# Kernel optimization log

Measured on AMD Instinct MI355X. Metric: run time of the kernel, lower is better.

Reference implementation:

```python
import jax, jax.numpy as jnp
import numpy as np

ALPHA = 0.1        # axis_aligned_projection threshold
NEG_INF = -1e30    # large negative used for masking (softmax-equivalent to -inf)


def axis_aligned_projection(x, alpha=ALPHA):
    x_abs = jnp.abs(x)
    max_vals = jnp.max(x_abs, axis=-1, keepdims=True)
    axis_weights = jnp.where(x_abs >= alpha * max_vals, x_abs, 0.0)
    return axis_weights * jnp.sign(x)


def setup_inputs() -> dict:
    key = jax.random.key(0)
    kq, kk, kv = jax.random.split(key, 3)
    B, L, H, E = 4, 2048, 8, 64
    S, D = L, E
    queries = jax.random.normal(kq, (B, L, H, E), dtype=jnp.float32)
    keys = jax.random.normal(kk, (B, S, H, E), dtype=jnp.float32)
    values = jax.random.normal(kv, (B, S, H, D), dtype=jnp.float32)
    # TriangularCausalMask: True strictly above the diagonal -> masked out
    causal = jnp.triu(jnp.ones((L, S), dtype=jnp.bool_), k=1)
    attn_mask = jnp.broadcast_to(causal[None, None], (B, 1, L, S))
    return {"queries": queries, "keys": keys, "values": values, "attn_mask": attn_mask}


def reference(queries, keys, values, attn_mask):
    B, L, H, E = queries.shape
    scale = 1.0 / jnp.sqrt(jnp.float32(E))
    q = axis_aligned_projection(queries)
    k = axis_aligned_projection(keys)
    # [B,H,L,S] dense scores (the module materializes the full matrix)
    scores = jnp.einsum('blhe,bshe->bhls', q, k)
    scores = jnp.where(attn_mask, NEG_INF, scores)
    A = jax.nn.softmax(scale * scores, axis=-1)  # dropout is identity in eval mode
    V = jnp.einsum('bhls,bshd->blhd', A, values)
    return V
```

## Files before the change

kernel.cpp:

```cpp
#include <hip/hip_runtime.h>
#include <hip/hip_bf16.h>
#include <stdint.h>

#define B_ 4
#define L_ 2048
#define H_ 8
#define E_ 64
#define ALPHA 0.1f
#define LOG2E 1.44269504088896f
#define QSCALE (0.125f * LOG2E)


typedef float f32x4 __attribute__((ext_vector_type(4)));
typedef short bf16x8 __attribute__((ext_vector_type(8)));
typedef short bf16x4 __attribute__((ext_vector_type(4)));
typedef uint32_t u32;
typedef unsigned short u16;
typedef u32 u32x2 __attribute__((ext_vector_type(2)));

__device__ __forceinline__ u16 f2bf(float f) {
    u32 x = __builtin_bit_cast(u32, f);
    u32 r = x + 0x7fffu + ((x >> 16) & 1u);
    return (u16)(r >> 16);
}

__device__ __forceinline__ u32 pk2bf(float a, float b) {
    u32 ua = __builtin_bit_cast(u32, a) + 0x8000u;
    u32 ub = __builtin_bit_cast(u32, b) + 0x8000u;
    return (ua >> 16) | (ub & 0xffff0000u);
}

__device__ __forceinline__ f32x4 mfma16x16x16bf16(bf16x4 a, bf16x4 b, f32x4 c) {
#if __has_builtin(__builtin_amdgcn_mfma_f32_16x16x16bf16_1k)
    return __builtin_amdgcn_mfma_f32_16x16x16bf16_1k(a, b, c, 0, 0, 0);
#elif __has_builtin(__builtin_amdgcn_mfma_f32_16x16x16_bf16)
    return __builtin_amdgcn_mfma_f32_16x16x16_bf16(a, b, c, 0, 0, 0);
#else
    f32x4 d;
    asm volatile("v_mfma_f32_16x16x16_bf16 %0, %1, %2, %3"
                 : "=v"(d) : "v"(a), "v"(b), "v"(c));
    return d;
#endif
}

__device__ __forceinline__ void dma16(const u16* g, u16* l) {
    __builtin_amdgcn_global_load_lds(
        (const __attribute__((address_space(1))) void*)g,
        (__attribute__((address_space(3))) void*)l, 16, 0, 0);
}

__global__ __launch_bounds__(256) void prep_kernel(const float* __restrict__ qin,
                                                   const float* __restrict__ kin,
                                                   const float* __restrict__ vin,
                                                   u16* __restrict__ qp,
                                                   u16* __restrict__ kp,
                                                   u16* __restrict__ vt) {
    __shared__ u16 tile[64][66];
    if (blockIdx.x < 4096) {
        const int RG = (B_ * L_ * H_) / 8;
        int wave = threadIdx.x >> 6, lane = threadIdx.x & 63;
        int g = blockIdx.x * 4 + wave;
        const float* src;
        u16* dst;
        int gr;
        float sc;
        bool isq;
        if (g < RG) { src = qin; dst = qp; gr = g; sc = QSCALE; isq = true; }
        else        { src = kin; dst = kp; gr = g - RG; sc = 1.0f; isq = false; }

        int rig = lane >> 3;
        int j = lane & 7;
        int c = j * 4;
        int row = gr * 8 + rig;

        const float* rp = src + (size_t)row * 64;
        float4 v0 = *(const float4*)(rp + c);
        float4 v1 = *(const float4*)(rp + c + 32);
        float f[8] = {v0.x, v0.y, v0.z, v0.w, v1.x, v1.y, v1.z, v1.w};

        float mx = 0.f;
#pragma unroll
        for (int i = 0; i < 8; ++i) mx = fmaxf(mx, fabsf(f[i]));
#pragma unroll
        for (int m = 1; m < 8; m <<= 1) mx = fmaxf(mx, __shfl_xor(mx, m));
        float thr = ALPHA * mx;

        u16 o[8];
#pragma unroll
        for (int i = 0; i < 8; ++i)
            o[i] = (fabsf(f[i]) >= thr) ? f2bf(f[i] * sc) : (u16)0;

        int b = row >> 14;
        int l = (row >> 3) & (L_ - 1);
        int h = row & 7;
        int e0, e1;
        if (isq) {
            e0 = c;
            e1 = c + 32;
        } else {
            int l7 = l & 7;
            e0 = (((j >> 1) ^ l7) << 3) + ((j & 1) << 2);
            e1 = ((((j >> 1) + 4) ^ l7) << 3) + ((j & 1) << 2);
        }
        u16* orow = dst + ((size_t)(b * H_ + h) * L_ + l) * 64;
        uint2 p0 = {(u32)o[0] | ((u32)o[1] << 16), (u32)o[2] | ((u32)o[3] << 16)};
        uint2 p1 = {(u32)o[4] | ((u32)o[5] << 16), (u32)o[6] | ((u32)o[7] << 16)};
        *(uint2*)(orow + e0) = p0;
        *(uint2*)(orow + e1) = p1;
    } else {
        int bx = blockIdx.x - 4096;
        int bh = bx >> 5, sblk = bx & 31;
        int b = bh >> 3, h = bh & 7;
        int t = threadIdx.x;
        int s0 = sblk * 64;

#pragma unroll
        for (int p = 0; p < 2; ++p) {
            int sl = p * 32 + (t >> 3);
            int c = (t & 7) * 4;
            const float* rp = vin + (((size_t)(b * L_ + s0 + sl)) * H_ + h) * 64;
            float4 a = *(const float4*)(rp + c);
            float4 bb = *(const float4*)(rp + c + 32);
            u32* d0 = (u32*)&tile[sl][c];
            d0[0] = (u32)f2bf(a.x) | ((u32)f2bf(a.y) << 16);
            d0[1] = (u32)f2bf(a.z) | ((u32)f2bf(a.w) << 16);
            u32* d1 = (u32*)&tile[sl][c + 32];
            d1[0] = (u32)f2bf(bb.x) | ((u32)f2bf(bb.y) << 16);
            d1[1] = (u32)f2bf(bb.z) | ((u32)f2bf(bb.w) << 16);
        }
        __syncthreads();
#pragma unroll
        for (int p = 0; p < 2; ++p) {
            int d = p * 32 + (t >> 3);
            int c16 = t & 7;
            int sc2 = c16 * 8;
            u16 o[8];
#pragma unroll
            for (int i = 0; i < 8; ++i) o[i] = tile[sc2 + i][d];
            u32 w0 = (u32)o[0] | ((u32)o[1] << 16);
            u32 w1 = (u32)o[2] | ((u32)o[3] << 16);
            u32 w2 = (u32)o[4] | ((u32)o[5] << 16);
            u32 w3 = (u32)o[6] | ((u32)o[7] << 16);
            uint4 val;
            if (d & 1) { val.x = w2; val.y = w3; val.z = w0; val.w = w1; }
            else       { val.x = w0; val.y = w1; val.z = w2; val.w = w3; }
            int pc = c16 ^ ((d >> 1) & 7);
            *(uint4*)(vt + ((size_t)(bh * 32 + sblk) * 64 + d) * 64 + pc * 8) = val;
        }
    }
}

__global__ __launch_bounds__(256, 4) void flash_kernel(const u16* __restrict__ Qp,
                                                       const u16* __restrict__ Kp,
                                                       const u16* __restrict__ Vt,
                                                       float* __restrict__ out) {
    __shared__ u16 kbuf[2][64 * 64];
    __shared__ u16 vbuf[2][64 * 64];
    int t = threadIdx.x;
    int wave = t >> 6, lane = t & 63;
    int bh = blockIdx.x & 31;
    int r5 = blockIdx.x >> 5;
    int g = r5 & 7, kr = r5 >> 3;
    int qq = (kr == 0) ? (31 - g) : (kr == 1) ? (16 + g) : (kr == 2) ? (15 - g) : g;
    int lo = lane & 15, quad = lane >> 4;
    int lo7 = lo & 7;
    int q0 = qq * 64 + wave * 16;
    int b = bh >> 3, h = bh & 7;

    int kc0 = (quad ^ lo7) << 3;
    int kc1 = ((quad + 4) ^ lo7) << 3;

    const u16* kTiles = Kp + (size_t)bh * L_ * 64;
    const u16* vTiles = Vt + (size_t)bh * 32 * 64 * 64;

    auto stage = [&](int sb, int buf) {
        const u16* kg = kTiles + (size_t)sb * 64;
        const u16* vg = vTiles + (size_t)(sb >> 6) * 64 * 64;
        u16* kl = kbuf[buf];
        u16* vl = vbuf[buf];
        for (int i = wave; i < 16; i += 4) {
            if (i < 8) dma16(kg + i * 512 + lane * 8, kl + i * 512);
            else       dma16(vg + (i - 8) * 512 + lane * 8, vl + (i - 8) * 512);
        }
    };

    const u16* qbase = Qp + ((size_t)bh * L_ + q0 + lo) * 64 + quad * 8;
    bf16x8 aQ0 = *(const bf16x8*)(qbase);
    bf16x8 aQ1 = *(const bf16x8*)(qbase + 32);
    asm volatile("" :: "v"(aQ0), "v"(aQ1));

    f32x4 o[4];
#pragma unroll
    for (int ni = 0; ni < 4; ++ni) o[ni] = (f32x4){0.f, 0.f, 0.f, 0.f};
    float ls = 0.f;

    auto tile_proc = [&](const u16* ks, const u16* vs) {
        bf16x8 k0[4], k1[4];
#pragma unroll
        for (int sub = 0; sub < 4; ++sub) {
            const u16* krow = ks + ((sub * 16 + lo) << 6);
            k0[sub] = *(const bf16x8*)(krow + kc0);
            k1[sub] = *(const bf16x8*)(krow + kc1);
        }
        bf16x4 vf[4][4];
#pragma unroll
        for (int sub = 0; sub < 4; ++sub) {
            int vsw = ((sub * 4 + quad) ^ lo) << 2;
#pragma unroll
            for (int ni = 0; ni < 4; ++ni)
                vf[sub][ni] = *(const bf16x4*)(vs + ((ni * 16 + lo) << 6) + vsw);
        }
        f32x4 S[4];
#pragma unroll
        for (int sub = 0; sub < 4; ++sub) {
            f32x4 acc = {0.f, 0.f, 0.f, 0.f};
            acc = __builtin_amdgcn_mfma_f32_16x16x32_bf16(k0[sub], aQ0, acc, 0, 0, 0);
            S[sub] = __builtin_amdgcn_mfma_f32_16x16x32_bf16(k1[sub], aQ1, acc, 0, 0, 0);
        }
        bf16x4 aP[4];
#pragma unroll
        for (int sub = 0; sub < 4; ++sub) {
            float P0 = __builtin_amdgcn_exp2f(S[sub][0]);
            float P1 = __builtin_amdgcn_exp2f(S[sub][1]);
            float P2 = __builtin_amdgcn_exp2f(S[sub][2]);
            float P3 = __builtin_amdgcn_exp2f(S[sub][3]);
            ls += (P0 + P1) + (P2 + P3);
            u32x2 pk = {pk2bf(P0, P1), pk2bf(P2, P3)};
            aP[sub] = __builtin_bit_cast(bf16x4, pk);
        }
#pragma unroll
        for (int sub = 0; sub < 4; ++sub)
#pragma unroll
            for (int ni = 0; ni < 4; ++ni)
                o[ni] = mfma16x16x16bf16(aP[sub], vf[sub][ni], o[ni]);
    };

    auto frag_proc = [&](const u16* ks, const u16* vs, int sub, bool diag) {
        const u16* krow = ks + ((sub * 16 + lo) << 6);
        bf16x8 k0 = *(const bf16x8*)(krow + kc0);
        bf16x8 k1 = *(const bf16x8*)(krow + kc1);
        f32x4 S = {0.f, 0.f, 0.f, 0.f};
        S = __builtin_amdgcn_mfma_f32_16x16x32_bf16(k0, aQ0, S, 0, 0, 0);
        S = __builtin_amdgcn_mfma_f32_16x16x32_bf16(k1, aQ1, S, 0, 0, 0);

        int vsw = ((sub * 4 + quad) ^ lo) << 2;
        bf16x4 vf[4];
#pragma unroll
        for (int ni = 0; ni < 4; ++ni)
            vf[ni] = *(const bf16x4*)(vs + ((ni * 16 + lo) << 6) + vsw);

        float P[4];
#pragma unroll
        for (int r = 0; r < 4; ++r) {
            float e = __builtin_amdgcn_exp2f(S[r]);
            P[r] = (diag && (quad * 4 + r > lo)) ? 0.f : e;
        }
        ls += (P[0] + P[1]) + (P[2] + P[3]);
        u32x2 pk = {pk2bf(P[0], P[1]), pk2bf(P[2], P[3])};
        bf16x4 aP = __builtin_bit_cast(bf16x4, pk);
#pragma unroll
        for (int ni = 0; ni < 4; ++ni)
            o[ni] = mfma16x16x16bf16(aP, vf[ni], o[ni]);
    };

    stage(0, 0);
    __syncthreads();

    for (int kt = 0; kt < qq; ++kt) {
        int cur = kt & 1;
        stage((kt + 1) << 6, cur ^ 1);
        tile_proc(kbuf[cur], vbuf[cur]);
        __syncthreads();
    }

    {
        int cur = qq & 1;
        const u16* ks = kbuf[cur];
        const u16* vs = vbuf[cur];
        for (int sub = 0; sub < wave; ++sub) frag_proc(ks, vs, sub, false);
        frag_proc(ks, vs, wave, true);
    }

    ls += __shfl_xor(ls, 16);
    ls += __shfl_xor(ls, 32);
#pragma unroll
    for (int r = 0; r < 4; ++r) {
        float lr = __shfl(ls, quad * 4 + r);
        float inv = 1.0f / lr;
        int q = q0 + quad * 4 + r;
        float* ob = out + (((size_t)(b * L_ + q)) * H_ + h) * 64 + lo;
        ob[0]  = o[0][r] * inv;
        ob[16] = o[1][r] * inv;
        ob[32] = o[2][r] * inv;
        ob[48] = o[3][r] * inv;
    }
}

extern "C" void kernel_launch(void* const* d_in, const int* in_sizes, int n_in,
                              void* d_out, int out_size, void* d_ws, size_t ws_size,
                              hipStream_t stream) {
    const float* q = (const float*)d_in[0];
    const float* k = (const float*)d_in[1];
    const float* v = (const float*)d_in[2];
    float* out = (float*)d_out;

    const size_t QSZ = (size_t)B_ * H_ * L_ * 64;
    u16* qp = (u16*)d_ws;
    u16* kp = qp + QSZ;
    u16* vt = kp + QSZ;

    prep_kernel<<<5120, 256, 0, stream>>>(q, k, v, qp, kp, vt);
    flash_kernel<<<1024, 256, 0, stream>>>(qp, kp, vt, out);
}
```

Measured before the change: 160.7 us.

## Pair complementary causal query tiles per block to share K/V staging

Each block now handles two query tiles, qa=31-p and qb=p, so every block does the same amount of causal work. The K/V tiles staged in shared memory are reused by both query tiles up to qb. This halves the grid to 512 blocks and drops launch bounds to 2 blocks per SM. The aim is to cut redundant K/V loads and balance the causal triangle, at the cost of more registers (two accumulators and two Q fragments) and lower occupancy.

```diff
diff --git a/kernel.cpp b/kernel.cpp
--- a/kernel.cpp
+++ b/kernel.cpp
@@ -150,7 +150,7 @@
     }
 }
 
-__global__ __launch_bounds__(256, 4) void flash_kernel(const u16* __restrict__ Qp,
+__global__ __launch_bounds__(256, 2) void flash_kernel(const u16* __restrict__ Qp,
                                                        const u16* __restrict__ Kp,
                                                        const u16* __restrict__ Vt,
                                                        float* __restrict__ out) {
@@ -158,13 +158,14 @@
     __shared__ u16 vbuf[2][64 * 64];
     int t = threadIdx.x;
     int wave = t >> 6, lane = t & 63;
-    int bh = blockIdx.x & 31;
-    int r5 = blockIdx.x >> 5;
-    int g = r5 & 7, kr = r5 >> 3;
-    int qq = (kr == 0) ? (31 - g) : (kr == 1) ? (16 + g) : (kr == 2) ? (15 - g) : g;
+    int bx = blockIdx.x;
+    int bh = bx & 31;
+    int pp = (bx >> 5) & 7;
+    int rr = bx >> 8;
+    int p = rr ? (15 - pp) : pp;
+    int qa = 31 - p, qb = p;
     int lo = lane & 15, quad = lane >> 4;
     int lo7 = lo & 7;
-    int q0 = qq * 64 + wave * 16;
     int b = bh >> 3, h = bh & 7;
 
     int kc0 = (quad ^ lo7) << 3;
@@ -173,9 +174,9 @@
     const u16* kTiles = Kp + (size_t)bh * L_ * 64;
     const u16* vTiles = Vt + (size_t)bh * 32 * 64 * 64;
 
-    auto stage = [&](int sb, int buf) {
-        const u16* kg = kTiles + (size_t)sb * 64;
-        const u16* vg = vTiles + (size_t)(sb >> 6) * 64 * 64;
+    auto stage = [&](int kt, int buf) {
+        const u16* kg = kTiles + (size_t)kt * 4096;
+        const u16* vg = vTiles + (size_t)kt * 4096;
         u16* kl = kbuf[buf];
         u16* vl = vbuf[buf];
         for (int i = wave; i < 16; i += 4) {
@@ -184,17 +185,23 @@
         }
     };
 
-    const u16* qbase = Qp + ((size_t)bh * L_ + q0 + lo) * 64 + quad * 8;
-    bf16x8 aQ0 = *(const bf16x8*)(qbase);
-    bf16x8 aQ1 = *(const bf16x8*)(qbase + 32);
-    asm volatile("" :: "v"(aQ0), "v"(aQ1));
-
-    f32x4 o[4];
-#pragma unroll
-    for (int ni = 0; ni < 4; ++ni) o[ni] = (f32x4){0.f, 0.f, 0.f, 0.f};
-    float ls = 0.f;
-
-    auto tile_proc = [&](const u16* ks, const u16* vs) {
+    const u16* qbA = Qp + ((size_t)bh * L_ + qa * 64 + wave * 16 + lo) * 64 + quad * 8;
+    bf16x8 aQ0a = *(const bf16x8*)(qbA);
+    bf16x8 aQ1a = *(const bf16x8*)(qbA + 32);
+    const u16* qbB = Qp + ((size_t)bh * L_ + qb * 64 + wave * 16 + lo) * 64 + quad * 8;
+    bf16x8 aQ0b = *(const bf16x8*)(qbB);
+    bf16x8 aQ1b = *(const bf16x8*)(qbB + 32);
+    asm volatile("" :: "v"(aQ0a), "v"(aQ1a), "v"(aQ0b), "v"(aQ1b));
+
+    f32x4 oA[4], oB[4];
+#pragma unroll
+    for (int ni = 0; ni < 4; ++ni) {
+        oA[ni] = (f32x4){0.f, 0.f, 0.f, 0.f};
+        oB[ni] = (f32x4){0.f, 0.f, 0.f, 0.f};
+    }
+    float lsA = 0.f, lsB = 0.f;
+
+    auto tile_proc = [&](const u16* ks, const u16* vs, bool doB) {
         bf16x8 k0[4], k1[4];
 #pragma unroll
         for (int sub = 0; sub < 4; ++sub) {
@@ -210,32 +217,60 @@
             for (int ni = 0; ni < 4; ++ni)
                 vf[sub][ni] = *(const bf16x4*)(vs + ((ni * 16 + lo) << 6) + vsw);
         }
-        f32x4 S[4];
+        f32x4 SA[4], SB[4];
 #pragma unroll
         for (int sub = 0; sub < 4; ++sub) {
             f32x4 acc = {0.f, 0.f, 0.f, 0.f};
-            acc = __builtin_amdgcn_mfma_f32_16x16x32_bf16(k0[sub], aQ0, acc, 0, 0, 0);
-            S[sub] = __builtin_amdgcn_mfma_f32_16x16x32_bf16(k1[sub], aQ1, acc, 0, 0, 0);
-        }
-        bf16x4 aP[4];
+            acc = __builtin_amdgcn_mfma_f32_16x16x32_bf16(k0[sub], aQ0a, acc, 0, 0, 0);
+            SA[sub] = __builtin_amdgcn_mfma_f32_16x16x32_bf16(k1[sub], aQ1a, acc, 0, 0, 0);
+        }
+        if (doB) {
+#pragma unroll
+            for (int sub = 0; sub < 4; ++sub) {
+                f32x4 acc = {0.f, 0.f, 0.f, 0.f};
+                acc = __builtin_amdgcn_mfma_f32_16x16x32_bf16(k0[sub], aQ0b, acc, 0, 0, 0);
+                SB[sub] = __builtin_amdgcn_mfma_f32_16x16x32_bf16(k1[sub], aQ1b, acc, 0, 0, 0);
+            }
+        }
+        bf16x4 aPA[4], aPB[4];
 #pragma unroll
         for (int sub = 0; sub < 4; ++sub) {
-            float P0 = __builtin_amdgcn_exp2f(S[sub][0]);
-            float P1 = __builtin_amdgcn_exp2f(S[sub][1]);
-            float P2 = __builtin_amdgcn_exp2f(S[sub][2]);
-            float P3 = __builtin_amdgcn_exp2f(S[sub][3]);
-            ls += (P0 + P1) + (P2 + P3);
+            float P0 = __builtin_amdgcn_exp2f(SA[sub][0]);
+            float P1 = __builtin_amdgcn_exp2f(SA[sub][1]);
+            float P2 = __builtin_amdgcn_exp2f(SA[sub][2]);
+            float P3 = __builtin_amdgcn_exp2f(SA[sub][3]);
+            lsA += (P0 + P1) + (P2 + P3);
             u32x2 pk = {pk2bf(P0, P1), pk2bf(P2, P3)};
-            aP[sub] = __builtin_bit_cast(bf16x4, pk);
+            aPA[sub] = __builtin_bit_cast(bf16x4, pk);
+        }
+        if (doB) {
+#pragma unroll
+            for (int sub = 0; sub < 4; ++sub) {
+                float P0 = __builtin_amdgcn_exp2f(SB[sub][0]);
+                float P1 = __builtin_amdgcn_exp2f(SB[sub][1]);
+                float P2 = __builtin_amdgcn_exp2f(SB[sub][2]);
+                float P3 = __builtin_amdgcn_exp2f(SB[sub][3]);
+                lsB += (P0 + P1) + (P2 + P3);
+                u32x2 pk = {pk2bf(P0, P1), pk2bf(P2, P3)};
+                aPB[sub] = __builtin_bit_cast(bf16x4, pk);
+            }
         }
 #pragma unroll
         for (int sub = 0; sub < 4; ++sub)
 #pragma unroll
             for (int ni = 0; ni < 4; ++ni)
-                o[ni] = mfma16x16x16bf16(aP[sub], vf[sub][ni], o[ni]);
+                oA[ni] = mfma16x16x16bf16(aPA[sub], vf[sub][ni], oA[ni]);
+        if (doB) {
+#pragma unroll
+            for (int sub = 0; sub < 4; ++sub)
+#pragma unroll
+                for (int ni = 0; ni < 4; ++ni)
+                    oB[ni] = mfma16x16x16bf16(aPB[sub], vf[sub][ni], oB[ni]);
+        }
     };
 
-    auto frag_proc = [&](const u16* ks, const u16* vs, int sub, bool diag) {
+    auto frag_proc = [&](const u16* ks, const u16* vs, int sub, bool diag,
+                         bf16x8 aQ0, bf16x8 aQ1, f32x4* o, float& ls) {
         const u16* krow = ks + ((sub * 16 + lo) << 6);
         bf16x8 k0 = *(const bf16x8*)(krow + kc0);
         bf16x8 k1 = *(const bf16x8*)(krow + kc1);
@@ -266,33 +301,62 @@
     stage(0, 0);
     __syncthreads();
 
-    for (int kt = 0; kt < qq; ++kt) {
+    int kt = 0;
+    for (; kt < qb; ++kt) {
         int cur = kt & 1;
-        stage((kt + 1) << 6, cur ^ 1);
-        tile_proc(kbuf[cur], vbuf[cur]);
+        stage(kt + 1, cur ^ 1);
+        tile_proc(kbuf[cur], vbuf[cur], true);
         __syncthreads();
     }
-
     {
-        int cur = qq & 1;
+        int cur = kt & 1;
+        stage(kt + 1, cur ^ 1);
+        tile_proc(kbuf[cur], vbuf[cur], false);
         const u16* ks = kbuf[cur];
         const u16* vs = vbuf[cur];
-        for (int sub = 0; sub < wave; ++sub) frag_proc(ks, vs, sub, false);
-        frag_proc(ks, vs, wave, true);
-    }
-
-    ls += __shfl_xor(ls, 16);
-    ls += __shfl_xor(ls, 32);
+        for (int sub = 0; sub < wave; ++sub)
+            frag_proc(ks, vs, sub, false, aQ0b, aQ1b, oB, lsB);
+        frag_proc(ks, vs, wave, true, aQ0b, aQ1b, oB, lsB);
+        __syncthreads();
+        ++kt;
+    }
+    for (; kt < qa; ++kt) {
+        int cur = kt & 1;
+        stage(kt + 1, cur ^ 1);
+        tile_proc(kbuf[cur], vbuf[cur], false);
+        __syncthreads();
+    }
+    {
+        int cur = qa & 1;
+        const u16* ks = kbuf[cur];
+        const u16* vs = vbuf[cur];
+        for (int sub = 0; sub < wave; ++sub)
+            frag_proc(ks, vs, sub, false, aQ0a, aQ1a, oA, lsA);
+        frag_proc(ks, vs, wave, true, aQ0a, aQ1a, oA, lsA);
+    }
+
+    lsA += __shfl_xor(lsA, 16);
+    lsA += __shfl_xor(lsA, 32);
+    lsB += __shfl_xor(lsB, 16);
+    lsB += __shfl_xor(lsB, 32);
 #pragma unroll
     for (int r = 0; r < 4; ++r) {
-        float lr = __shfl(ls, quad * 4 + r);
-        float inv = 1.0f / lr;
-        int q = q0 + quad * 4 + r;
-        float* ob = out + (((size_t)(b * L_ + q)) * H_ + h) * 64 + lo;
-        ob[0]  = o[0][r] * inv;
-        ob[16] = o[1][r] * inv;
-        ob[32] = o[2][r] * inv;
-        ob[48] = o[3][r] * inv;
+        float lrA = __shfl(lsA, quad * 4 + r);
+        float invA = 1.0f / lrA;
+        int qArow = qa * 64 + wave * 16 + quad * 4 + r;
+        float* obA = out + (((size_t)(b * L_ + qArow)) * H_ + h) * 64 + lo;
+        obA[0]  = oA[0][r] * invA;
+        obA[16] = oA[1][r] * invA;
+        obA[32] = oA[2][r] * invA;
+        obA[48] = oA[3][r] * invA;
+        float lrB = __shfl(lsB, quad * 4 + r);
+        float invB = 1.0f / lrB;
+        int qBrow = qb * 64 + wave * 16 + quad * 4 + r;
+        float* obB = out + (((size_t)(b * L_ + qBrow)) * H_ + h) * 64 + lo;
+        obB[0]  = oB[0][r] * invB;
+        obB[16] = oB[1][r] * invB;
+        obB[32] = oB[2][r] * invB;
+        obB[48] = oB[3][r] * invB;
     }
 }
 
@@ -310,5 +374,5 @@
     u16* vt = kp + QSZ;
 
     prep_kernel<<<5120, 256, 0, stream>>>(q, k, v, qp, kp, vt);
-    flash_kernel<<<1024, 256, 0, stream>>>(qp, kp, vt, out);
-}
+    flash_kernel<<<512, 256, 0, stream>>>(qp, kp, vt, out);
+}
```

Measured after the change: 162.7 us. About the same (+1.3%).
